# Optimization experiments

Measured on AMD Instinct MI355X. Metric: run time of the kernel, lower is better.

The kernel has to match this reference:

```python
import jax, jax.numpy as jnp
import numpy as np

V, D, L, H, S, B = 50257, 768, 12, 12, 1024, 2
DH = D // H          # 64
F4 = 4 * D           # 3072
EPS = 1e-5


def _ln(x, g, b):
    m = jnp.mean(x, axis=-1, keepdims=True)
    v = jnp.mean((x - m) ** 2, axis=-1, keepdims=True)
    return (x - m) * jax.lax.rsqrt(v + EPS) * g + b


def setup_inputs() -> dict:
    key = jax.random.key(0)
    ks = jax.random.split(key, 16)
    n = lambda k, shape: jax.random.normal(k, shape, jnp.float32) * 0.02
    return {
        "tokens": jax.random.randint(ks[0], (B, S), 0, V),
        "tok_emb": n(ks[1], (V, D)),
        "pos_emb": n(ks[2], (S, D)),
        "ln1_g": jnp.ones((L, D), jnp.float32), "ln1_b": jnp.zeros((L, D), jnp.float32),
        "wq": n(ks[3], (L, D, D)), "bq": jnp.zeros((L, D), jnp.float32),
        "wk": n(ks[4], (L, D, D)), "bk": jnp.zeros((L, D), jnp.float32),
        "wv": n(ks[5], (L, D, D)), "bv": jnp.zeros((L, D), jnp.float32),
        "wo": n(ks[6], (L, D, D)), "bo": jnp.zeros((L, D), jnp.float32),
        "ln2_g": jnp.ones((L, D), jnp.float32), "ln2_b": jnp.zeros((L, D), jnp.float32),
        "w1": n(ks[7], (L, D, F4)), "b1": jnp.zeros((L, F4), jnp.float32),
        "w2": n(ks[8], (L, F4, D)), "b2": jnp.zeros((L, D), jnp.float32),
        "fn_g": jnp.ones((D,), jnp.float32), "fn_b": jnp.zeros((D,), jnp.float32),
        "head_w": n(ks[9], (D, V)), "head_b": jnp.zeros((V,), jnp.float32),
    }


def reference(tokens, tok_emb, pos_emb, ln1_g, ln1_b, wq, bq, wk, bk, wv, bv,
              wo, bo, ln2_g, ln2_b, w1, b1, w2, b2, fn_g, fn_b, head_w, head_b):
    b_, s_ = tokens.shape
    x = tok_emb[tokens] + pos_emb[:s_]                       # [B,S,D]
    causal = jnp.tril(jnp.ones((s_, s_), bool))              # allow j <= i
    scale = 1.0 / np.sqrt(DH)

    def block(x, p):
        g1, c1, Wq, Bq, Wk, Bk, Wv, Bv_, Wo, Bo, g2, c2, W1, B1, W2, B2 = p
        h = _ln(x, g1, c1)
        q = (h @ Wq + Bq).reshape(b_, s_, H, DH)
        k = (h @ Wk + Bk).reshape(b_, s_, H, DH)
        v = (h @ Wv + Bv_).reshape(b_, s_, H, DH)
        scores = jnp.einsum('bqhd,bkhd->bhqk', q, k) * scale  # [B,H,S,S]
        scores = jnp.where(causal, scores, -jnp.inf)
        attn = jax.nn.softmax(scores, axis=-1)
        o = jnp.einsum('bhqk,bkhd->bqhd', attn, v).reshape(b_, s_, D)
        x = x + (o @ Wo + Bo)
        h2 = _ln(x, g2, c2)
        ff = jax.nn.gelu(h2 @ W1 + B1, approximate=False) @ W2 + B2
        return x + ff, None

    x, _ = jax.lax.scan(block, x, (ln1_g, ln1_b, wq, bq, wk, bk, wv, bv,
                                   wo, bo, ln2_g, ln2_b, w1, b1, w2, b2))
    return _ln(x, fn_g, fn_b) @ head_w + head_b               # [B,S,V]
```

## Files before the change

kernel.cpp:

```cpp
#include <hip/hip_runtime.h>

typedef __bf16 bf16;
typedef bf16 bf16x8 __attribute__((ext_vector_type(8)));
typedef float f32x4 __attribute__((ext_vector_type(4)));

#define SQ  1024
#define DIM 768
#define NH  12
#define NL  12
#define F4  3072
#define NPADV 50304
#define NVOC  50257

__device__ __forceinline__ void async16(bf16* lds, const bf16* g) {
  __builtin_amdgcn_global_load_lds(
      (const __attribute__((address_space(1))) unsigned int*)g,
      (__attribute__((address_space(3))) unsigned int*)lds, 16, 0, 0);
}

__global__ __launch_bounds__(256) void embed_kernel(
    const int* __restrict__ tokens, const float* __restrict__ tok_emb,
    const float* __restrict__ pos_emb, float* __restrict__ x) {
  int row = blockIdx.x;
  int s   = row & (SQ - 1);
  int tok = tokens[row];
  for (int i = threadIdx.x; i < DIM; i += 256)
    x[(size_t)row * DIM + i] = tok_emb[(size_t)tok * DIM + i] + pos_emb[(size_t)s * DIM + i];
}

__global__ __launch_bounds__(256) void ln_kernel(
    const float* __restrict__ x, const float* __restrict__ g,
    const float* __restrict__ b, bf16* __restrict__ out) {
  int row = blockIdx.x;
  const float* xr = x + (size_t)row * DIM;
  int t = threadIdx.x;
  float v0 = xr[t], v1 = xr[t + 256], v2 = xr[t + 512];
  float s  = v0 + v1 + v2;
  float sq = v0 * v0 + v1 * v1 + v2 * v2;
#pragma unroll
  for (int off = 32; off; off >>= 1) {
    s  += __shfl_xor(s, off);
    sq += __shfl_xor(sq, off);
  }
  __shared__ float rs[4], rq[4];
  int wid = t >> 6, lane = t & 63;
  if (lane == 0) { rs[wid] = s; rq[wid] = sq; }
  __syncthreads();
  float S = rs[0] + rs[1] + rs[2] + rs[3];
  float Q = rq[0] + rq[1] + rq[2] + rq[3];
  float mean = S * (1.0f / DIM);
  float var  = Q * (1.0f / DIM) - mean * mean;
  float rstd = rsqrtf(var + 1e-5f);
  bf16* orow = out + (size_t)row * DIM;
  orow[t]       = (bf16)((v0 - mean) * rstd * g[t]       + b[t]);
  orow[t + 256] = (bf16)((v1 - mean) * rstd * g[t + 256] + b[t + 256]);
  orow[t + 512] = (bf16)((v2 - mean) * rstd * g[t + 512] + b[t + 512]);
}

__global__ __launch_bounds__(256) void tconv_kernel(
    const float* __restrict__ src, bf16* __restrict__ dst,
    int K, int N, size_t s_stride, size_t d_stride) {
  __shared__ float tile[32][33];
  const float* s = src + blockIdx.z * s_stride;
  bf16* d = dst + blockIdx.z * d_stride;
  int n0 = blockIdx.x * 32, k0 = blockIdx.y * 32;
  int tx = threadIdx.x & 31, ty = threadIdx.x >> 5;
#pragma unroll
  for (int r = 0; r < 32; r += 8) {
    int n = n0 + tx;
    tile[ty + r][tx] = (n < N) ? s[(size_t)(k0 + ty + r) * N + n] : 0.f;
  }
  __syncthreads();
#pragma unroll
  for (int r = 0; r < 32; r += 8)
    d[(size_t)(n0 + ty + r) * K + k0 + tx] = (bf16)tile[tx][ty + r];
}

__global__ __launch_bounds__(256) void packb_kernel(
    const float* __restrict__ bq, const float* __restrict__ bk,
    const float* __restrict__ bv, float* __restrict__ qkvb) {
  int l = blockIdx.x, t = threadIdx.x;
  for (int i = t; i < DIM; i += 256) {
    qkvb[(size_t)l * 2304 + i]        = bq[(size_t)l * DIM + i];
    qkvb[(size_t)l * 2304 + 768 + i]  = bk[(size_t)l * DIM + i];
    qkvb[(size_t)l * 2304 + 1536 + i] = bv[(size_t)l * DIM + i];
  }
}

template <int BM, int DEPTH, bool GELU_, bool RESID, bool OUTBF, bool NT>
__global__ __launch_bounds__(BM == 128 ? 512 : 256) void gemm_bt(
    const bf16* __restrict__ A, const bf16* __restrict__ BT,
    const float* __restrict__ bias, const float* __restrict__ resid,
    float* __restrict__ outF, bf16* __restrict__ outB,
    int M, int N, int K) {
  constexpr int BK = 64;
  constexpr int WAVES = (BM == 128) ? 8 : 4;
  constexpr int BROW = 128 / WAVES;
  constexpr int NB = BROW / 8;
  constexpr int EPLD = 68;
  constexpr size_t GBYTES = (size_t)DEPTH * (BM + 128) * BK * 2;
  constexpr size_t EBYTES = NT ? (size_t)WAVES * 32 * EPLD * 4 : 0;
  constexpr size_t SBYTES = (EBYTES > GBYTES) ? EBYTES : GBYTES;
  __shared__ __align__(16) char smem[SBYTES];

  const int gx = gridDim.x;
  const int lid = blockIdx.y * gx + blockIdx.x;
  const int q8 = (gx * gridDim.y) >> 3;
  const int work = (lid & 7) * q8 + (lid >> 3);
  const int m0 = (work % gx) * BM, n0 = (work / gx) * 128;

  const int t = threadIdx.x, w = t >> 6, lane = t & 63;
  const int wm = (w >> 1) * 32, wn = (w & 1) * 64;
  const int row16 = lane & 15, kg = lane >> 4;
  const int srow = lane >> 3;
  const int scol = ((lane & 7) ^ srow) * 8;
  f32x4 acc[2][4] = {};

  const bf16* Abase = A  + (size_t)(m0 + w * 16 + srow) * K + scol;
  const bf16* Bbase = BT + (size_t)(n0 + w * BROW + srow) * K + scol;

  auto stage = [&](int buf, int k0) {
    bf16* as = (bf16*)smem + (size_t)buf * BM * BK;
    bf16* bs = (bf16*)smem + (size_t)DEPTH * BM * BK + (size_t)buf * 128 * BK;
#pragma unroll
    for (int i = 0; i < 2; i++)
      async16(as + (w * 16 + i * 8) * BK, Abase + (size_t)(i * 8) * K + k0);
#pragma unroll
    for (int i = 0; i < NB; i++)
      async16(bs + (w * BROW + i * 8) * BK, Bbase + (size_t)(i * 8) * K + k0);
  };

  const int nk = K / BK;
  stage(0, 0);
  if constexpr (DEPTH == 3) stage(1, BK);
  for (int ki = 0; ki < nk; ki++) {
    const int cur = ki % DEPTH;
    const bf16* Ac = (const bf16*)smem + (size_t)cur * BM * BK;
    const bf16* Bc = (const bf16*)smem + (size_t)DEPTH * BM * BK + (size_t)cur * 128 * BK;
    if (ki + DEPTH - 1 < nk) {
      stage((ki + DEPTH - 1) % DEPTH, (ki + DEPTH - 1) * BK);
      if constexpr (DEPTH == 3)      asm volatile("s_waitcnt vmcnt(12)" ::: "memory");
      else if constexpr (BM == 128)  asm volatile("s_waitcnt vmcnt(4)"  ::: "memory");
      else                           asm volatile("s_waitcnt vmcnt(6)"  ::: "memory");
    } else if (DEPTH == 3 && ki + 1 < nk) {
      asm volatile("s_waitcnt vmcnt(6)" ::: "memory");
    } else {
      asm volatile("s_waitcnt vmcnt(0)" ::: "memory");
    }
    __builtin_amdgcn_s_barrier();
    __builtin_amdgcn_sched_barrier(0);
    const int psw = row16 & 7;
#pragma unroll
    for (int kk = 0; kk < 2; kk++) {
      const int pc = ((kk * 4 + kg) ^ psw) * 8;
      bf16x8 af[2], bfv[4];
#pragma unroll
      for (int i = 0; i < 2; i++)
        af[i] = *(const bf16x8*)(&Ac[(wm + i * 16 + row16) * BK + pc]);
#pragma unroll
      for (int j = 0; j < 4; j++)
        bfv[j] = *(const bf16x8*)(&Bc[(wn + j * 16 + row16) * BK + pc]);
#pragma unroll
      for (int i = 0; i < 2; i++)
#pragma unroll
        for (int j = 0; j < 4; j++)
          acc[i][j] = __builtin_amdgcn_mfma_f32_16x16x32_bf16(af[i], bfv[j], acc[i][j], 0, 0, 0);
    }
    if (ki + 1 < nk) {
      __builtin_amdgcn_s_barrier();
      __builtin_amdgcn_sched_barrier(0);
    }
  }

  if constexpr (NT) {
    __syncthreads();
    float* ws = (float*)smem + (size_t)w * 32 * EPLD;
#pragma unroll
    for (int i = 0; i < 2; i++)
#pragma unroll
      for (int j = 0; j < 4; j++) {
        int col = n0 + wn + j * 16 + row16;
        float bi = (col < N) ? bias[col] : 0.f;
#pragma unroll
        for (int r = 0; r < 4; r++)
          ws[(i * 16 + kg * 4 + r) * EPLD + j * 16 + row16] = acc[i][j][r] + bi;
      }
    const int lr = lane >> 4, lc = (lane & 15) * 4;
#pragma unroll
    for (int p = 0; p < 8; p++) {
      int row = m0 + (w >> 1) * 32 + p * 4 + lr;
      int col = n0 + (w & 1) * 64 + lc;
      f32x4 v = *(const f32x4*)&ws[(p * 4 + lr) * EPLD + lc];
      float* dst = outF + (size_t)row * N + col;
      if (col + 3 < N) {
        __builtin_nontemporal_store(v, (f32x4*)dst);
      } else {
#pragma unroll
        for (int e = 0; e < 4; e++)
          if (col + e < N) __builtin_nontemporal_store(v[e], dst + e);
      }
    }
  } else {
#pragma unroll
    for (int i = 0; i < 2; i++)
#pragma unroll
      for (int j = 0; j < 4; j++) {
        int col = n0 + wn + j * 16 + row16;
        if (col < N) {
          float bi = bias[col];
#pragma unroll
          for (int r = 0; r < 4; r++) {
            int row = m0 + wm + i * 16 + kg * 4 + r;
            float val = acc[i][j][r] + bi;
            if constexpr (GELU_) val = 0.5f * val * (1.0f + erff(val * 0.70710678f));
            if constexpr (RESID) val += resid[(size_t)row * N + col];
            if constexpr (OUTBF) outB[(size_t)row * N + col] = (bf16)val;
            else                 outF[(size_t)row * N + col] = val;
          }
        }
      }
  }
}

__global__ __launch_bounds__(512) void fattn_kernel(
    const bf16* __restrict__ qkv, bf16* __restrict__ o) {
  constexpr int LP = 72;
  constexpr int LDQ = 2304;
  __shared__ bf16 Ks[64 * LP];
  __shared__ bf16 Vt[64 * LP];
  __shared__ bf16 Ps[8][16 * LP];

  const int qt = 7 - (blockIdx.x & 7);
  const int hb = blockIdx.x >> 3;
  const int h  = hb % NH;
  const int b  = hb / NH;
  const int t = threadIdx.x;
  const int w = t >> 6, lane = t & 63;
  const int row16 = lane & 15, kg = lane >> 4;

  const bf16* kbase = qkv + 768  + (size_t)(b * SQ) * LDQ + h * 64;
  const bf16* vbase = qkv + 1536 + (size_t)(b * SQ) * LDQ + h * 64;

  const int wq0  = qt * 128 + w * 16;
  const int qrow = wq0 + row16;
  const bf16* qptr = qkv + (size_t)(b * SQ + qrow) * LDQ + h * 64;
  const bf16x8 qf0 = *(const bf16x8*)(qptr + kg * 8);
  const bf16x8 qf1 = *(const bf16x8*)(qptr + 32 + kg * 8);

  f32x4 oacc[4] = {};
  float mrow[4] = {-1e30f, -1e30f, -1e30f, -1e30f};
  float lrow[4] = {0.f, 0.f, 0.f, 0.f};
  const int myq = wq0 + kg * 4;
  const int ntiles = 2 * qt + 2;

  for (int jb0 = 0; jb0 < ntiles; jb0++) {
    const int j0 = jb0 * 64;
    __syncthreads();
    {
      int key = t >> 3, d8 = (t & 7) * 8;
      *(uint4*)(&Ks[key * LP + d8]) =
          *(const uint4*)(kbase + (size_t)(j0 + key) * LDQ + d8);
      bf16x8 vv = *(const bf16x8*)(vbase + (size_t)(j0 + key) * LDQ + d8);
      int kc = key >> 3, kl = key & 7;
#pragma unroll
      for (int e = 0; e < 8; e++) {
        int d = d8 + e;
        Vt[d * LP + ((kc ^ (d >> 3)) << 3) + kl] = vv[e];
      }
    }
    __syncthreads();

    if (j0 > wq0 + 15) continue;

    f32x4 sacc[4];
    __builtin_amdgcn_s_setprio(1);
#pragma unroll
    for (int jb = 0; jb < 4; jb++) {
      bf16x8 kf0 = *(const bf16x8*)(&Ks[(jb * 16 + row16) * LP + kg * 8]);
      bf16x8 kf1 = *(const bf16x8*)(&Ks[(jb * 16 + row16) * LP + 32 + kg * 8]);
      f32x4 sa = {};
      sa = __builtin_amdgcn_mfma_f32_16x16x32_bf16(qf0, kf0, sa, 0, 0, 0);
      sa = __builtin_amdgcn_mfma_f32_16x16x32_bf16(qf1, kf1, sa, 0, 0, 0);
      sacc[jb] = sa;
    }
    __builtin_amdgcn_s_setprio(0);

    constexpr float SC = 0.125f * 1.44269504f;
    if (j0 + 63 > wq0) {
#pragma unroll
      for (int jb = 0; jb < 4; jb++) {
        int keyg = j0 + jb * 16 + row16;
#pragma unroll
        for (int r = 0; r < 4; r++)
          sacc[jb][r] = (keyg <= myq + r) ? sacc[jb][r] * SC : -1e30f;
      }
    } else {
#pragma unroll
      for (int jb = 0; jb < 4; jb++)
#pragma unroll
        for (int r = 0; r < 4; r++)
          sacc[jb][r] *= SC;
    }

    float p[4][4];
#pragma unroll
    for (int r = 0; r < 4; r++) {
      float mx = fmaxf(fmaxf(sacc[0][r], sacc[1][r]), fmaxf(sacc[2][r], sacc[3][r]));
      mx = fmaxf(mx, __shfl_xor(mx, 1));
      mx = fmaxf(mx, __shfl_xor(mx, 2));
      mx = fmaxf(mx, __shfl_xor(mx, 4));
      mx = fmaxf(mx, __shfl_xor(mx, 8));
      float mn = fmaxf(mrow[r], mx);
      float al = exp2f(mrow[r] - mn);
      mrow[r] = mn;
      float ls = 0.f;
#pragma unroll
      for (int jb = 0; jb < 4; jb++) {
        float pv = exp2f(sacc[jb][r] - mn);
        p[jb][r] = pv;
        ls += pv;
      }
      ls += __shfl_xor(ls, 1);
      ls += __shfl_xor(ls, 2);
      ls += __shfl_xor(ls, 4);
      ls += __shfl_xor(ls, 8);
      lrow[r] = lrow[r] * al + ls;
#pragma unroll
      for (int dt = 0; dt < 4; dt++) oacc[dt][r] *= al;
    }

    bf16* pw = &Ps[w][0];
#pragma unroll
    for (int jb = 0; jb < 4; jb++)
#pragma unroll
      for (int r = 0; r < 4; r++)
        pw[(kg * 4 + r) * LP + jb * 16 + row16] = (bf16)p[jb][r];

    bf16x8 pf0 = *(const bf16x8*)(&pw[row16 * LP + kg * 8]);
    bf16x8 pf1 = *(const bf16x8*)(&pw[row16 * LP + 32 + kg * 8]);

    __builtin_amdgcn_s_setprio(1);
#pragma unroll
    for (int dt = 0; dt < 4; dt++) {
      int drow = dt * 16 + row16;
      int sw = (drow >> 3) & 7;
      bf16x8 vf0 = *(const bf16x8*)(&Vt[drow * LP + ((kg ^ sw) << 3)]);
      bf16x8 vf1 = *(const bf16x8*)(&Vt[drow * LP + (((4 + kg) ^ sw) << 3)]);
      oacc[dt] = __builtin_amdgcn_mfma_f32_16x16x32_bf16(pf0, vf0, oacc[dt], 0, 0, 0);
      oacc[dt] = __builtin_amdgcn_mfma_f32_16x16x32_bf16(pf1, vf1, oacc[dt], 0, 0, 0);
    }
    __builtin_amdgcn_s_setprio(0);
  }

  bf16* obase = o + (size_t)(b * SQ + wq0 + kg * 4) * DIM + h * 64;
#pragma unroll
  for (int r = 0; r < 4; r++) {
    float inv = 1.0f / lrow[r];
#pragma unroll
    for (int dt = 0; dt < 4; dt++)
      obase[(size_t)r * DIM + dt * 16 + row16] = (bf16)(oacc[dt][r] * inv);
  }
}

template <bool GELU_, bool RESID, bool OUTBF>
__global__ __launch_bounds__(256) void gemm_kernel(
    const bf16* __restrict__ A, const float* __restrict__ W,
    const float* __restrict__ bias, const float* __restrict__ resid,
    float* __restrict__ outF, bf16* __restrict__ outB,
    int M, int N, int K) {
  constexpr int BM = 128, BN = 128, BK = 32, LDP = 40;
  __shared__ bf16 As[BM * LDP];
  __shared__ bf16 Bs[BN * LDP];
  int m0 = blockIdx.y * BM;
  int n0 = blockIdx.x * BN;
  int t = threadIdx.x;
  int wid = t >> 6, lane = t & 63;
  int wm = (wid >> 1) * 64, wn = (wid & 1) * 64;
  int row16 = lane & 15, kg = lane >> 4;
  f32x4 acc[4][4] = {};
  bool edge = (n0 + BN > N);

  for (int k0 = 0; k0 < K; k0 += BK) {
#pragma unroll
    for (int r2 = 0; r2 < 2; r2++) {
      int idx = t + r2 * 256;
      int row = idx >> 2, c8 = (idx & 3) * 8;
      uint4 va = *reinterpret_cast<const uint4*>(A + (size_t)(m0 + row) * K + k0 + c8);
      *reinterpret_cast<uint4*>(&As[row * LDP + c8]) = va;
    }
#pragma unroll
    for (int r = 0; r < 8; r++) {
      int idx = t + r * 256;
      int n = idx & 127, kp = idx >> 7;
      int kk = kp * 2;
      float w0 = 0.f, w1 = 0.f;
      if (!edge || (n0 + n) < N) {
        w0 = W[(size_t)(k0 + kk) * N + n0 + n];
        w1 = W[(size_t)(k0 + kk + 1) * N + n0 + n];
      }
      bf16 b0 = (bf16)w0, b1 = (bf16)w1;
      union { bf16 b[2]; unsigned int u; } pk;
      pk.b[0] = b0; pk.b[1] = b1;
      *reinterpret_cast<unsigned int*>(&Bs[n * LDP + kk]) = pk.u;
    }
    __syncthreads();
    bf16x8 af[4], bfv[4];
#pragma unroll
    for (int i = 0; i < 4; i++)
      af[i] = *reinterpret_cast<const bf16x8*>(&As[(wm + i * 16 + row16) * LDP + kg * 8]);
#pragma unroll
    for (int j = 0; j < 4; j++)
      bfv[j] = *reinterpret_cast<const bf16x8*>(&Bs[(wn + j * 16 + row16) * LDP + kg * 8]);
#pragma unroll
    for (int i = 0; i < 4; i++)
#pragma unroll
      for (int j = 0; j < 4; j++)
        acc[i][j] = __builtin_amdgcn_mfma_f32_16x16x32_bf16(af[i], bfv[j], acc[i][j], 0, 0, 0);
    __syncthreads();
  }

  int crow = (lane >> 4) * 4;
  int ccol = lane & 15;
#pragma unroll
  for (int i = 0; i < 4; i++)
#pragma unroll
    for (int j = 0; j < 4; j++) {
      int col = n0 + wn + j * 16 + ccol;
      if (col < N) {
        float bi = bias[col];
#pragma unroll
        for (int r = 0; r < 4; r++) {
          int row = m0 + wm + i * 16 + crow + r;
          float val = acc[i][j][r] + bi;
          if constexpr (GELU_) val = 0.5f * val * (1.0f + erff(val * 0.70710678f));
          if constexpr (RESID) val += resid[(size_t)row * N + col];
          if constexpr (OUTBF) outB[(size_t)row * N + col] = (bf16)val;
          else                 outF[(size_t)row * N + col] = val;
        }
      }
    }
}

__global__ __launch_bounds__(256) void fattn_legacy_kernel(
    const bf16* __restrict__ q, const bf16* __restrict__ k,
    const bf16* __restrict__ v, bf16* __restrict__ o) {
  constexpr int LP = 72;
  __shared__ bf16 Ks[64 * LP];
  __shared__ bf16 Vt[64 * LP];
  __shared__ bf16 Ps[4][16 * LP];
  const int qt = blockIdx.x & 15;
  const int h  = (blockIdx.x >> 4) % NH;
  const int b  = blockIdx.x / (16 * NH);
  const int t = threadIdx.x;
  const int w = t >> 6, lane = t & 63;
  const int row16 = lane & 15, kg = lane >> 4;
  const bf16* kbase = k + (size_t)(b * SQ) * DIM + h * 64;
  const bf16* vbase = v + (size_t)(b * SQ) * DIM + h * 64;
  const int qrow = qt * 64 + w * 16 + row16;
  const bf16* qptr = q + (size_t)(b * SQ + qrow) * DIM + h * 64;
  const bf16x8 qf0 = *(const bf16x8*)(qptr + kg * 8);
  const bf16x8 qf1 = *(const bf16x8*)(qptr + 32 + kg * 8);
  f32x4 oacc[4] = {};
  float mrow[4] = {-1e30f, -1e30f, -1e30f, -1e30f};
  float lrow[4] = {0.f, 0.f, 0.f, 0.f};
  const int myq = qt * 64 + w * 16 + kg * 4;
  for (int jb0 = 0; jb0 <= qt; jb0++) {
    const int j0 = jb0 * 64;
    __syncthreads();
#pragma unroll
    for (int it = 0; it < 2; it++) {
      int idx = t + it * 256;
      int key = idx >> 3, d8 = (idx & 7) * 8;
      *(uint4*)(&Ks[key * LP + d8]) = *(const uint4*)(kbase + (size_t)(j0 + key) * DIM + d8);
    }
#pragma unroll
    for (int it = 0; it < 2; it++) {
      int idx = t + it * 256;
      int key = idx >> 3, d8 = (idx & 7) * 8;
      bf16x8 vv = *(const bf16x8*)(vbase + (size_t)(j0 + key) * DIM + d8);
      int kc = key >> 3, kl = key & 7;
#pragma unroll
      for (int e = 0; e < 8; e++) {
        int d = d8 + e;
        Vt[d * LP + ((kc ^ (d >> 3)) << 3) + kl] = vv[e];
      }
    }
    __syncthreads();
    f32x4 sacc[4];
#pragma unroll
    for (int jb = 0; jb < 4; jb++) {
      bf16x8 kf0 = *(const bf16x8*)(&Ks[(jb * 16 + row16) * LP + kg * 8]);
      bf16x8 kf1 = *(const bf16x8*)(&Ks[(jb * 16 + row16) * LP + 32 + kg * 8]);
      f32x4 sa = {};
      sa = __builtin_amdgcn_mfma_f32_16x16x32_bf16(qf0, kf0, sa, 0, 0, 0);
      sa = __builtin_amdgcn_mfma_f32_16x16x32_bf16(qf1, kf1, sa, 0, 0, 0);
      sacc[jb] = sa;
    }
    constexpr float SC = 0.125f * 1.44269504f;
    if (jb0 == qt) {
#pragma unroll
      for (int jb = 0; jb < 4; jb++) {
        int keyg = j0 + jb * 16 + row16;
#pragma unroll
        for (int r = 0; r < 4; r++)
          sacc[jb][r] = (keyg <= myq + r) ? sacc[jb][r] * SC : -1e30f;
      }
    } else {
#pragma unroll
      for (int jb = 0; jb < 4; jb++)
#pragma unroll
        for (int r = 0; r < 4; r++)
          sacc[jb][r] *= SC;
    }
    float p[4][4];
#pragma unroll
    for (int r = 0; r < 4; r++) {
      float mx = fmaxf(fmaxf(sacc[0][r], sacc[1][r]), fmaxf(sacc[2][r], sacc[3][r]));
      mx = fmaxf(mx, __shfl_xor(mx, 1));
      mx = fmaxf(mx, __shfl_xor(mx, 2));
      mx = fmaxf(mx, __shfl_xor(mx, 4));
      mx = fmaxf(mx, __shfl_xor(mx, 8));
      float mn = fmaxf(mrow[r], mx);
      float al = exp2f(mrow[r] - mn);
      mrow[r] = mn;
      float ls = 0.f;
#pragma unroll
      for (int jb = 0; jb < 4; jb++) {
        float pv = exp2f(sacc[jb][r] - mn);
        p[jb][r] = pv;
        ls += pv;
      }
      ls += __shfl_xor(ls, 1);
      ls += __shfl_xor(ls, 2);
      ls += __shfl_xor(ls, 4);
      ls += __shfl_xor(ls, 8);
      lrow[r] = lrow[r] * al + ls;
#pragma unroll
      for (int dt = 0; dt < 4; dt++) oacc[dt][r] *= al;
    }
    bf16* pw = &Ps[w][0];
#pragma unroll
    for (int jb = 0; jb < 4; jb++)
#pragma unroll
      for (int r = 0; r < 4; r++)
        pw[(kg * 4 + r) * LP + jb * 16 + row16] = (bf16)p[jb][r];
    bf16x8 pf0 = *(const bf16x8*)(&pw[row16 * LP + kg * 8]);
    bf16x8 pf1 = *(const bf16x8*)(&pw[row16 * LP + 32 + kg * 8]);
#pragma unroll
    for (int dt = 0; dt < 4; dt++) {
      int drow = dt * 16 + row16;
      int sw = (drow >> 3) & 7;
      bf16x8 vf0 = *(const bf16x8*)(&Vt[drow * LP + ((kg ^ sw) << 3)]);
      bf16x8 vf1 = *(const bf16x8*)(&Vt[drow * LP + (((4 + kg) ^ sw) << 3)]);
      oacc[dt] = __builtin_amdgcn_mfma_f32_16x16x32_bf16(pf0, vf0, oacc[dt], 0, 0, 0);
      oacc[dt] = __builtin_amdgcn_mfma_f32_16x16x32_bf16(pf1, vf1, oacc[dt], 0, 0, 0);
    }
  }
  bf16* obase = o + (size_t)(b * SQ + qt * 64 + w * 16 + kg * 4) * DIM + h * 64;
#pragma unroll
  for (int r = 0; r < 4; r++) {
    float inv = 1.0f / lrow[r];
#pragma unroll
    for (int dt = 0; dt < 4; dt++)
      obase[(size_t)r * DIM + dt * 16 + row16] = (bf16)(oacc[dt][r] * inv);
  }
}

extern "C" void kernel_launch(void* const* d_in, const int* in_sizes, int n_in,
                              void* d_out, int out_size, void* d_ws, size_t ws_size,
                              hipStream_t stream) {
  const int*   tokens  = (const int*)  d_in[0];
  const float* tok_emb = (const float*)d_in[1];
  const float* pos_emb = (const float*)d_in[2];
  const float* ln1_g   = (const float*)d_in[3];
  const float* ln1_b   = (const float*)d_in[4];
  const float* wq      = (const float*)d_in[5];
  const float* bq      = (const float*)d_in[6];
  const float* wk      = (const float*)d_in[7];
  const float* bk      = (const float*)d_in[8];
  const float* wv      = (const float*)d_in[9];
  const float* bv      = (const float*)d_in[10];
  const float* wo      = (const float*)d_in[11];
  const float* bo      = (const float*)d_in[12];
  const float* ln2_g   = (const float*)d_in[13];
  const float* ln2_b   = (const float*)d_in[14];
  const float* w1      = (const float*)d_in[15];
  const float* b1      = (const float*)d_in[16];
  const float* w2      = (const float*)d_in[17];
  const float* b2      = (const float*)d_in[18];
  const float* fn_g    = (const float*)d_in[19];
  const float* fn_b    = (const float*)d_in[20];
  const float* head_w  = (const float*)d_in[21];
  const float* head_b  = (const float*)d_in[22];
  float* out = (float*)d_out;

  const int ROWS = 2 * SQ;
  char* p = (char*)d_ws;
  float* x   = (float*)p;  p += (size_t)ROWS * DIM * 4;
  bf16*  h   = (bf16*)p;   p += (size_t)ROWS * DIM * 2;
  bf16*  qkv = (bf16*)p;   p += (size_t)ROWS * 2304 * 2;
  bf16*  ao  = (bf16*)p;   p += (size_t)ROWS * DIM * 2;
  bf16*  mid = (bf16*)p;   p += (size_t)ROWS * F4  * 2;
  bf16*  WqkvT = (bf16*)p; p += (size_t)NL * 2304 * DIM * 2;
  bf16*  WoT   = (bf16*)p; p += (size_t)NL * DIM * DIM * 2;
  bf16*  W1T   = (bf16*)p; p += (size_t)NL * F4 * DIM * 2;
  bf16*  W2T   = (bf16*)p; p += (size_t)NL * DIM * F4 * 2;
  bf16*  WhT   = (bf16*)p; p += (size_t)NPADV * DIM * 2;
  float* qkvb  = (float*)p; p += (size_t)NL * 2304 * 4;
  size_t need = (size_t)(p - (char*)d_ws);

  embed_kernel<<<ROWS, 256, 0, stream>>>(tokens, tok_emb, pos_emb, x);

  if (ws_size >= need) {
    {
      dim3 gdd(DIM / 32, DIM / 32, NL);
      size_t ss = (size_t)DIM * DIM, ds = (size_t)2304 * DIM;
      tconv_kernel<<<gdd, 256, 0, stream>>>(wq, WqkvT,                       DIM, DIM, ss, ds);
      tconv_kernel<<<gdd, 256, 0, stream>>>(wk, WqkvT + (size_t)768  * DIM,  DIM, DIM, ss, ds);
      tconv_kernel<<<gdd, 256, 0, stream>>>(wv, WqkvT + (size_t)1536 * DIM,  DIM, DIM, ss, ds);
      tconv_kernel<<<gdd, 256, 0, stream>>>(wo, WoT, DIM, DIM, ss, ss);
      dim3 g1(F4 / 32, DIM / 32, NL);
      tconv_kernel<<<g1, 256, 0, stream>>>(w1, W1T, DIM, F4, (size_t)DIM * F4, (size_t)F4 * DIM);
      dim3 g2(DIM / 32, F4 / 32, NL);
      tconv_kernel<<<g2, 256, 0, stream>>>(w2, W2T, F4, DIM, (size_t)F4 * DIM, (size_t)DIM * F4);
      dim3 gh(NPADV / 32, DIM / 32, 1);
      tconv_kernel<<<gh, 256, 0, stream>>>(head_w, WhT, DIM, NVOC, 0, 0);
      packb_kernel<<<NL, 256, 0, stream>>>(bq, bk, bv, qkvb);
    }

    dim3 gQKV(32, 2304 / 128);
    dim3 gD(32, DIM / 128);
    dim3 gF(32, F4 / 128);
    dim3 gV(16, NPADV / 128);

    for (int l = 0; l < NL; l++) {
      ln_kernel<<<ROWS, 256, 0, stream>>>(x, ln1_g + l * DIM, ln1_b + l * DIM, h);
      gemm_bt<64, 2, false, false, true, false><<<gQKV, 256, 0, stream>>>(
          h, WqkvT + (size_t)l * 2304 * DIM, qkvb + (size_t)l * 2304,
          nullptr, nullptr, qkv, ROWS, 2304, DIM);
      fattn_kernel<<<2 * NH * (SQ / 128), 512, 0, stream>>>(qkv, ao);
      gemm_bt<64, 3, false, true, false, false><<<gD, 256, 0, stream>>>(
          ao, WoT + (size_t)l * DIM * DIM, bo + l * DIM, x, x, nullptr, ROWS, DIM, DIM);
      ln_kernel<<<ROWS, 256, 0, stream>>>(x, ln2_g + l * DIM, ln2_b + l * DIM, h);
      gemm_bt<64, 2, true, false, true, false><<<gF, 256, 0, stream>>>(
          h, W1T + (size_t)l * F4 * DIM, b1 + l * F4, nullptr, nullptr, mid, ROWS, F4, DIM);
      gemm_bt<64, 3, false, true, false, false><<<gD, 256, 0, stream>>>(
          mid, W2T + (size_t)l * DIM * F4, b2 + l * DIM, x, x, nullptr, ROWS, DIM, F4);
    }
    ln_kernel<<<ROWS, 256, 0, stream>>>(x, fn_g, fn_b, h);
    gemm_bt<128, 2, false, false, false, true><<<gV, 512, 0, stream>>>(
        h, WhT, head_b, nullptr, out, nullptr, ROWS, NVOC, DIM);
  } else {
    char* q2 = (char*)d_ws;
    float* xf  = (float*)q2; q2 += (size_t)ROWS * DIM * 4;
    bf16*  hf  = (bf16*)q2;  q2 += (size_t)ROWS * DIM * 2;
    bf16*  qb2 = (bf16*)q2;  q2 += (size_t)ROWS * DIM * 2;
    bf16*  kb2 = (bf16*)q2;  q2 += (size_t)ROWS * DIM * 2;
    bf16*  vb2 = (bf16*)q2;  q2 += (size_t)ROWS * DIM * 2;
    bf16*  ao2 = (bf16*)q2;  q2 += (size_t)ROWS * DIM * 2;
    bf16*  mi2 = (bf16*)q2;  q2 += (size_t)ROWS * F4  * 2;
    dim3 gD(DIM / 128, ROWS / 128);
    dim3 gF(F4 / 128, ROWS / 128);
    dim3 gV((NVOC + 127) / 128, ROWS / 128);
    for (int l = 0; l < NL; l++) {
      size_t wo_off = (size_t)l * DIM * DIM;
      ln_kernel<<<ROWS, 256, 0, stream>>>(xf, ln1_g + l * DIM, ln1_b + l * DIM, hf);
      gemm_kernel<false, false, true><<<gD, 256, 0, stream>>>(
          hf, wq + wo_off, bq + l * DIM, nullptr, nullptr, qb2, ROWS, DIM, DIM);
      gemm_kernel<false, false, true><<<gD, 256, 0, stream>>>(
          hf, wk + wo_off, bk + l * DIM, nullptr, nullptr, kb2, ROWS, DIM, DIM);
      gemm_kernel<false, false, true><<<gD, 256, 0, stream>>>(
          hf, wv + wo_off, bv + l * DIM, nullptr, nullptr, vb2, ROWS, DIM, DIM);
      fattn_legacy_kernel<<<2 * NH * (SQ / 64), 256, 0, stream>>>(qb2, kb2, vb2, ao2);
      gemm_kernel<false, true, false><<<gD, 256, 0, stream>>>(
          ao2, wo + wo_off, bo + l * DIM, xf, xf, nullptr, ROWS, DIM, DIM);
      ln_kernel<<<ROWS, 256, 0, stream>>>(xf, ln2_g + l * DIM, ln2_b + l * DIM, hf);
      gemm_kernel<true, false, true><<<gF, 256, 0, stream>>>(
          hf, w1 + (size_t)l * DIM * F4, b1 + l * F4, nullptr, nullptr, mi2, ROWS, F4, DIM);
      gemm_kernel<false, true, false><<<gD, 256, 0, stream>>>(
          mi2, w2 + (size_t)l * F4 * DIM, b2 + l * DIM, xf, xf, nullptr, ROWS, DIM, F4);
    }
    ln_kernel<<<ROWS, 256, 0, stream>>>(xf, fn_g, fn_b, hf);
    gemm_kernel<false, false, false><<<gV, 256, 0, stream>>>(
        hf, head_w, head_b, nullptr, out, nullptr, ROWS, NVOC, DIM);
  }
}
```

Before: 1.957 ms.

## Double flash-attention key tile to 128 keys per iteration

Each iteration of the attention kernel now loads a 128-key tile of K and V into shared memory instead of 64, halving the number of loop iterations and block-wide barriers. Score, softmax and PV loops are widened to 8 key subtiles, with a wider padded V-transpose and P buffer. The per-warp skip of fully masked tiles is removed, so warps do some extra masked work in the diagonal tile. LDS use and register pressure both grow.

```diff
diff --git a/kernel.cpp b/kernel.cpp
--- a/kernel.cpp
+++ b/kernel.cpp
@@ -224,11 +224,13 @@
 
 __global__ __launch_bounds__(512) void fattn_kernel(
     const bf16* __restrict__ qkv, bf16* __restrict__ o) {
-  constexpr int LP = 72;
+  constexpr int LP  = 72;
+  constexpr int LPV = 136;
+  constexpr int LPP = 136;
   constexpr int LDQ = 2304;
-  __shared__ bf16 Ks[64 * LP];
-  __shared__ bf16 Vt[64 * LP];
-  __shared__ bf16 Ps[8][16 * LP];
+  __shared__ bf16 Ks[128 * LP];
+  __shared__ bf16 Vt[64 * LPV];
+  __shared__ bf16 Ps[8][16 * LPP];
 
   const int qt = 7 - (blockIdx.x & 7);
   const int hb = blockIdx.x >> 3;
@@ -251,13 +253,15 @@
   float mrow[4] = {-1e30f, -1e30f, -1e30f, -1e30f};
   float lrow[4] = {0.f, 0.f, 0.f, 0.f};
   const int myq = wq0 + kg * 4;
-  const int ntiles = 2 * qt + 2;
+  const int ntiles = qt + 1;
 
   for (int jb0 = 0; jb0 < ntiles; jb0++) {
-    const int j0 = jb0 * 64;
+    const int j0 = jb0 * 128;
     __syncthreads();
-    {
-      int key = t >> 3, d8 = (t & 7) * 8;
+#pragma unroll
+    for (int it = 0; it < 2; it++) {
+      int idx = t + it * 512;
+      int key = idx >> 3, d8 = (idx & 7) * 8;
       *(uint4*)(&Ks[key * LP + d8]) =
           *(const uint4*)(kbase + (size_t)(j0 + key) * LDQ + d8);
       bf16x8 vv = *(const bf16x8*)(vbase + (size_t)(j0 + key) * LDQ + d8);
@@ -265,17 +269,15 @@
 #pragma unroll
       for (int e = 0; e < 8; e++) {
         int d = d8 + e;
-        Vt[d * LP + ((kc ^ (d >> 3)) << 3) + kl] = vv[e];
+        Vt[d * LPV + ((kc ^ (d >> 3)) << 3) + kl] = vv[e];
       }
     }
     __syncthreads();
 
-    if (j0 > wq0 + 15) continue;
-
-    f32x4 sacc[4];
+    f32x4 sacc[8];
     __builtin_amdgcn_s_setprio(1);
 #pragma unroll
-    for (int jb = 0; jb < 4; jb++) {
+    for (int jb = 0; jb < 8; jb++) {
       bf16x8 kf0 = *(const bf16x8*)(&Ks[(jb * 16 + row16) * LP + kg * 8]);
       bf16x8 kf1 = *(const bf16x8*)(&Ks[(jb * 16 + row16) * LP + 32 + kg * 8]);
       f32x4 sa = {};
@@ -286,9 +288,9 @@
     __builtin_amdgcn_s_setprio(0);
 
     constexpr float SC = 0.125f * 1.44269504f;
-    if (j0 + 63 > wq0) {
-#pragma unroll
-      for (int jb = 0; jb < 4; jb++) {
+    if (j0 + 127 > wq0) {
+#pragma unroll
+      for (int jb = 0; jb < 8; jb++) {
         int keyg = j0 + jb * 16 + row16;
 #pragma unroll
         for (int r = 0; r < 4; r++)
@@ -296,16 +298,18 @@
       }
     } else {
 #pragma unroll
-      for (int jb = 0; jb < 4; jb++)
+      for (int jb = 0; jb < 8; jb++)
 #pragma unroll
         for (int r = 0; r < 4; r++)
           sacc[jb][r] *= SC;
     }
 
-    float p[4][4];
+    float p[8][4];
 #pragma unroll
     for (int r = 0; r < 4; r++) {
-      float mx = fmaxf(fmaxf(sacc[0][r], sacc[1][r]), fmaxf(sacc[2][r], sacc[3][r]));
+      float mx = sacc[0][r];
+#pragma unroll
+      for (int jb = 1; jb < 8; jb++) mx = fmaxf(mx, sacc[jb][r]);
       mx = fmaxf(mx, __shfl_xor(mx, 1));
       mx = fmaxf(mx, __shfl_xor(mx, 2));
       mx = fmaxf(mx, __shfl_xor(mx, 4));
@@ -315,7 +319,7 @@
       mrow[r] = mn;
       float ls = 0.f;
 #pragma unroll
-      for (int jb = 0; jb < 4; jb++) {
+      for (int jb = 0; jb < 8; jb++) {
         float pv = exp2f(sacc[jb][r] - mn);
         p[jb][r] = pv;
         ls += pv;
@@ -331,23 +335,26 @@
 
     bf16* pw = &Ps[w][0];
 #pragma unroll
-    for (int jb = 0; jb < 4; jb++)
+    for (int jb = 0; jb < 8; jb++)
 #pragma unroll
       for (int r = 0; r < 4; r++)
-        pw[(kg * 4 + r) * LP + jb * 16 + row16] = (bf16)p[jb][r];
-
-    bf16x8 pf0 = *(const bf16x8*)(&pw[row16 * LP + kg * 8]);
-    bf16x8 pf1 = *(const bf16x8*)(&pw[row16 * LP + 32 + kg * 8]);
+        pw[(kg * 4 + r) * LPP + jb * 16 + row16] = (bf16)p[jb][r];
+
+    bf16x8 pf[4];
+#pragma unroll
+    for (int m = 0; m < 4; m++)
+      pf[m] = *(const bf16x8*)(&pw[row16 * LPP + m * 32 + kg * 8]);
 
     __builtin_amdgcn_s_setprio(1);
 #pragma unroll
     for (int dt = 0; dt < 4; dt++) {
       int drow = dt * 16 + row16;
-      int sw = (drow >> 3) & 7;
-      bf16x8 vf0 = *(const bf16x8*)(&Vt[drow * LP + ((kg ^ sw) << 3)]);
-      bf16x8 vf1 = *(const bf16x8*)(&Vt[drow * LP + (((4 + kg) ^ sw) << 3)]);
-      oacc[dt] = __builtin_amdgcn_mfma_f32_16x16x32_bf16(pf0, vf0, oacc[dt], 0, 0, 0);
-      oacc[dt] = __builtin_amdgcn_mfma_f32_16x16x32_bf16(pf1, vf1, oacc[dt], 0, 0, 0);
+      int sw = drow >> 3;
+#pragma unroll
+      for (int m = 0; m < 4; m++) {
+        bf16x8 vf = *(const bf16x8*)(&Vt[drow * LPV + (((m * 4 + kg) ^ sw) << 3)]);
+        oacc[dt] = __builtin_amdgcn_mfma_f32_16x16x32_bf16(pf[m], vf, oacc[dt], 0, 0, 0);
+      }
     }
     __builtin_amdgcn_s_setprio(0);
   }
```

Result: faster. 1.886 ms (-3.7%).
